# Performance work log

Hardware: AMD Instinct MI355X
Metric: run time of the kernel (lower is better)

## Reference

```python
import jax, jax.numpy as jnp
import numpy as np

B, T, E, H, HD, FF = 2, 2048, 1024, 16, 64, 4096
LN_EPS = 1e-5


def _ln(x, g, b):
    mu = jnp.mean(x, axis=-1, keepdims=True)
    var = jnp.var(x, axis=-1, keepdims=True)
    return (x - mu) * jax.lax.rsqrt(var + LN_EPS) * g + b


def setup_inputs() -> dict:
    key = jax.random.key(0)
    ks = jax.random.split(key, 8)
    s = 0.02
    return {
        "x": jax.random.normal(ks[0], (B, T, E), jnp.float32),
        "Wq": jax.random.normal(ks[1], (H, E, HD), jnp.float32) * s,
        "Wk": jax.random.normal(ks[2], (H, E, HD), jnp.float32) * s,
        "Wv": jax.random.normal(ks[3], (H, E, HD), jnp.float32) * s,
        "Wproj": jax.random.normal(ks[4], (E, E), jnp.float32) * s,
        "bproj": jnp.zeros((E,), jnp.float32),
        "W1": jax.random.normal(ks[5], (E, FF), jnp.float32) * s,
        "b1": jnp.zeros((FF,), jnp.float32),
        "W2": jax.random.normal(ks[6], (FF, E), jnp.float32) * s,
        "b2": jnp.zeros((E,), jnp.float32),
        "g1": jnp.ones((E,), jnp.float32),
        "be1": jnp.zeros((E,), jnp.float32),
        "g2": jnp.ones((E,), jnp.float32),
        "be2": jnp.zeros((E,), jnp.float32),
    }


def reference(x, Wq, Wk, Wv, Wproj, bproj, W1, b1, W2, b2, g1, be1, g2, be2):
    # --- pre-LN multi-head causal self-attention (dropout = eval/identity) ---
    h = _ln(x, g1, be1)  # [B,T,E]
    q = jnp.einsum('btd,hde->bhte', h, Wq)  # [B,H,T,HD]
    k = jnp.einsum('btd,hde->bhte', h, Wk)
    v = jnp.einsum('btd,hde->bhte', h, Wv)
    # NOTE: original code scales by C**-0.5 where C = embedding_dim (not head_size)
    scale = E ** (-0.5)
    wei = jnp.einsum('bhqe,bhke->bhqk', q, k) * scale  # [B,H,T,T]
    causal = jnp.tril(jnp.ones((T, T), dtype=bool))
    wei = jnp.where(causal, wei, -jnp.inf)
    attn = jax.nn.softmax(wei, axis=-1)
    o = jnp.einsum('bhqk,bhke->bhqe', attn, v)  # [B,H,T,HD]
    o = o.transpose(0, 2, 1, 3).reshape(B, T, E)  # concat heads
    o = o @ Wproj + bproj
    x = x + o
    # --- ReLU FFN ---
    h2 = _ln(x, g2, be2)
    f = jax.nn.relu(h2 @ W1 + b1) @ W2 + b2
    return x + f
```

## Files before the change

### kernel.cpp

```cpp
#include <hip/hip_runtime.h>
#include <hip/hip_bf16.h>
#include <stdint.h>

#define T_SEQ 2048
#define E_DIM 1024
#define H_NUM 16
#define HD_DIM 64
#define FF_DIM 4096
#define B_NUM 2
#define N_TOK (B_NUM * T_SEQ)

typedef unsigned short ushort_t;
typedef __bf16 bf16x8 __attribute__((ext_vector_type(8)));
typedef float f32x4 __attribute__((ext_vector_type(4)));

__device__ __forceinline__ float bf2f(ushort_t u) {
    return __uint_as_float(((unsigned)u) << 16);
}
__device__ __forceinline__ ushort_t f2bf(float f) {
    unsigned u = __float_as_uint(f);
    u += 0x7fffu + ((u >> 16) & 1u);
    return (ushort_t)(u >> 16);
}
__device__ __forceinline__ float bflo(unsigned u) { return __uint_as_float(u << 16); }
__device__ __forceinline__ float bfhi(unsigned u) { return __uint_as_float(u & 0xffff0000u); }

__device__ __forceinline__ void async_copy16(const ushort_t* g, ushort_t* l) {
    __builtin_amdgcn_global_load_lds(
        (__attribute__((address_space(1))) uint32_t*)(ushort_t*)g,
        (__attribute__((address_space(3))) uint32_t*)l, 16, 0, 0);
}

__global__ __launch_bounds__(256) void ln_kernel(const float* __restrict__ x,
                                                 const float* __restrict__ g,
                                                 const float* __restrict__ be,
                                                 ushort_t* __restrict__ out) {
    __shared__ float red[8];
    const int row = blockIdx.x, tid = threadIdx.x;
    const float* xr = x + (size_t)row * E_DIM;
    float4 v = ((const float4*)xr)[tid];
    float s = v.x + v.y + v.z + v.w;
    float sq = v.x * v.x + v.y * v.y + v.z * v.z + v.w * v.w;
    for (int off = 32; off; off >>= 1) {
        s += __shfl_xor(s, off);
        sq += __shfl_xor(sq, off);
    }
    const int wid = tid >> 6, lane = tid & 63;
    if (lane == 0) { red[wid] = s; red[4 + wid] = sq; }
    __syncthreads();
    s = red[0] + red[1] + red[2] + red[3];
    sq = red[4] + red[5] + red[6] + red[7];
    const float mean = s * (1.0f / E_DIM);
    const float var = sq * (1.0f / E_DIM) - mean * mean;
    const float rstd = rsqrtf(var + 1e-5f);
    float4 gv = ((const float4*)g)[tid];
    float4 bv = ((const float4*)be)[tid];
    unsigned o0 = f2bf((v.x - mean) * rstd * gv.x + bv.x);
    unsigned o1 = f2bf((v.y - mean) * rstd * gv.y + bv.y);
    unsigned o2 = f2bf((v.z - mean) * rstd * gv.z + bv.z);
    unsigned o3 = f2bf((v.w - mean) * rstd * gv.w + bv.w);
    uint2 w;
    w.x = o0 | (o1 << 16);
    w.y = o2 | (o3 << 16);
    ((uint2*)(out + (size_t)row * E_DIM))[tid] = w;
}

__global__ __launch_bounds__(256) void reduce_ln_kernel(const ushort_t* __restrict__ p0,
                                                        const ushort_t* __restrict__ p1,
                                                        const float* __restrict__ x,
                                                        const float* __restrict__ bias,
                                                        const float* __restrict__ g,
                                                        const float* __restrict__ be,
                                                        float* __restrict__ x1,
                                                        ushort_t* __restrict__ h2) {
    __shared__ float red[8];
    const int row = blockIdx.x, tid = threadIdx.x;
    uint2 u0 = ((const uint2*)(p0 + (size_t)row * E_DIM))[tid];
    uint2 u1 = ((const uint2*)(p1 + (size_t)row * E_DIM))[tid];
    float4 xv = ((const float4*)(x + (size_t)row * E_DIM))[tid];
    float4 bv = ((const float4*)bias)[tid];
    float4 v;
    v.x = xv.x + bv.x + bflo(u0.x) + bflo(u1.x);
    v.y = xv.y + bv.y + bfhi(u0.x) + bfhi(u1.x);
    v.z = xv.z + bv.z + bflo(u0.y) + bflo(u1.y);
    v.w = xv.w + bv.w + bfhi(u0.y) + bfhi(u1.y);
    ((float4*)(x1 + (size_t)row * E_DIM))[tid] = v;
    float s = v.x + v.y + v.z + v.w;
    float sq = v.x * v.x + v.y * v.y + v.z * v.z + v.w * v.w;
    for (int off = 32; off; off >>= 1) {
        s += __shfl_xor(s, off);
        sq += __shfl_xor(sq, off);
    }
    const int wid = tid >> 6, lane = tid & 63;
    if (lane == 0) { red[wid] = s; red[4 + wid] = sq; }
    __syncthreads();
    s = red[0] + red[1] + red[2] + red[3];
    sq = red[4] + red[5] + red[6] + red[7];
    const float mean = s * (1.0f / E_DIM);
    const float var = sq * (1.0f / E_DIM) - mean * mean;
    const float rstd = rsqrtf(var + 1e-5f);
    float4 gv = ((const float4*)g)[tid];
    float4 ev = ((const float4*)be)[tid];
    unsigned o0 = f2bf((v.x - mean) * rstd * gv.x + ev.x);
    unsigned o1 = f2bf((v.y - mean) * rstd * gv.y + ev.y);
    unsigned o2 = f2bf((v.z - mean) * rstd * gv.z + ev.z);
    unsigned o3 = f2bf((v.w - mean) * rstd * gv.w + ev.w);
    uint2 w;
    w.x = o0 | (o1 << 16);
    w.y = o2 | (o3 << 16);
    ((uint2*)(h2 + (size_t)row * E_DIM))[tid] = w;
}

__global__ __launch_bounds__(256) void reduce_out_kernel(const ushort_t* __restrict__ p0,
                                                         const ushort_t* __restrict__ p1,
                                                         const float* __restrict__ x1,
                                                         const float* __restrict__ bias,
                                                         float* __restrict__ out) {
    const int row = blockIdx.x, tid = threadIdx.x;
    uint2 u0 = ((const uint2*)(p0 + (size_t)row * E_DIM))[tid];
    uint2 u1 = ((const uint2*)(p1 + (size_t)row * E_DIM))[tid];
    float4 xv = ((const float4*)(x1 + (size_t)row * E_DIM))[tid];
    float4 bv = ((const float4*)bias)[tid];
    float4 v;
    v.x = xv.x + bv.x + bflo(u0.x) + bflo(u1.x);
    v.y = xv.y + bv.y + bfhi(u0.x) + bfhi(u1.x);
    v.z = xv.z + bv.z + bflo(u0.y) + bflo(u1.y);
    v.w = xv.w + bv.w + bfhi(u0.y) + bfhi(u1.y);
    ((float4*)(out + (size_t)row * E_DIM))[tid] = v;
}

__global__ __launch_bounds__(256) void transpose_all_kernel(const float* __restrict__ Wq,
                                                            const float* __restrict__ Wk,
                                                            const float* __restrict__ Wv,
                                                            const float* __restrict__ Wproj,
                                                            const float* __restrict__ W1,
                                                            const float* __restrict__ W2,
                                                            ushort_t* __restrict__ WqkvT,
                                                            ushort_t* __restrict__ WprojT,
                                                            ushort_t* __restrict__ W1T,
                                                            ushort_t* __restrict__ W2T) {
    __shared__ ushort_t tile[32][33];
    const int id = blockIdx.x;
    const float* in;
    ushort_t* out;
    int R, C, r0, c0;
    if (id < 3072) {
        const int z = id >> 6, rem = id & 63;
        const int m = z >> 4, hh = z & 15;
        in = ((m == 0) ? Wq : ((m == 1) ? Wk : Wv)) + (size_t)hh * E_DIM * HD_DIM;
        out = WqkvT + (size_t)(m * E_DIM + hh * HD_DIM) * E_DIM;
        R = E_DIM; C = HD_DIM;
        c0 = (rem & 1) * 32; r0 = (rem >> 1) * 32;
    } else if (id < 4096) {
        const int i = id - 3072;
        in = Wproj; out = WprojT; R = E_DIM; C = E_DIM;
        c0 = (i & 31) * 32; r0 = (i >> 5) * 32;
    } else if (id < 8192) {
        const int i = id - 4096;
        in = W1; out = W1T; R = E_DIM; C = FF_DIM;
        c0 = (i & 127) * 32; r0 = (i >> 7) * 32;
    } else {
        const int i = id - 8192;
        in = W2; out = W2T; R = FF_DIM; C = E_DIM;
        c0 = (i & 31) * 32; r0 = (i >> 5) * 32;
    }
    const int tx = threadIdx.x, ty = threadIdx.y;
#pragma unroll
    for (int i = 0; i < 32; i += 8) tile[ty + i][tx] = f2bf(in[(size_t)(r0 + ty + i) * C + (c0 + tx)]);
    __syncthreads();
#pragma unroll
    for (int i = 0; i < 32; i += 8) out[(size_t)(c0 + ty + i) * R + (r0 + tx)] = tile[tx][ty + i];
}

template <int MODE, int BK>
__global__ __launch_bounds__(256) void gemm_bt(const ushort_t* __restrict__ A,
                                               const ushort_t* __restrict__ BT,
                                               const float* __restrict__ bias,
                                               const float* __restrict__ resid,
                                               void* __restrict__ C0,
                                               ushort_t* __restrict__ C1,
                                               ushort_t* __restrict__ C2,
                                               int M, int N, int K, int lda) {
    __shared__ __align__(16) ushort_t lds_a[2][128 * BK];
    __shared__ __align__(16) ushort_t lds_b[2][128 * BK];
    const int tid = threadIdx.x;
    const int id = blockIdx.y * gridDim.x + blockIdx.x;
    const int band = id & 7, within = id >> 3;
    const int rpb = gridDim.y >> 3;
    const int by = band * rpb + (within % rpb);
    const int bx = within / rpb;
    const int m0 = by * 128, n0 = bx * 128;
    const int koff = blockIdx.z * K;
    const int wave = tid >> 6, lane = tid & 63;
    const int wm = (wave >> 1) * 64, wn = (wave & 1) * 64;
    const int quad = lane >> 4, l16 = lane & 15;
    f32x4 acc[4][4] = {};

    const int nk = K / BK;
    auto stage = [&](int kt, int buf) {
        const int k0 = koff + kt * BK;
#pragma unroll
        for (int it = 0; it < BK / 16; ++it) {
            const int ci = it * 256 + tid;
            const int kk = ci >> 9;
            const int rem = ci & 511;
            const int r = rem >> 2, kc = rem & 3;
            const int gk = k0 + kk * 32 + kc * 8;
            async_copy16(A + (size_t)(m0 + r) * lda + gk, &lds_a[buf][ci * 8]);
            async_copy16(BT + (size_t)(n0 + r) * lda + gk, &lds_b[buf][ci * 8]);
        }
    };
    stage(0, 0);

#pragma unroll 1
    for (int kt = 0; kt < nk; ++kt) {
        __syncthreads();
        if (kt + 1 < nk) stage(kt + 1, (kt + 1) & 1);
        const ushort_t* la = lds_a[kt & 1];
        const ushort_t* lb = lds_b[kt & 1];
#pragma unroll
        for (int kk = 0; kk < BK / 32; ++kk) {
            const ushort_t* lak = la + kk * 4096;
            const ushort_t* lbk = lb + kk * 4096;
            bf16x8 af[4], bfr[4];
#pragma unroll
            for (int i = 0; i < 4; i++) af[i] = *(const bf16x8*)&lak[(wm + i * 16 + l16) * 32 + quad * 8];
#pragma unroll
            for (int i = 0; i < 4; i++) bfr[i] = *(const bf16x8*)&lbk[(wn + i * 16 + l16) * 32 + quad * 8];
#pragma unroll
            for (int im = 0; im < 4; im++)
#pragma unroll
                for (int in = 0; in < 4; in++)
                    acc[im][in] = __builtin_amdgcn_mfma_f32_16x16x32_bf16(af[im], bfr[in], acc[im][in], 0, 0, 0);
        }
    }

    ushort_t* pc = nullptr;
    if (MODE == 3) pc = (blockIdx.z == 0) ? (ushort_t*)C0 : C1;
#pragma unroll
    for (int im = 0; im < 4; im++) {
#pragma unroll
        for (int in = 0; in < 4; in++) {
            const int col = n0 + wn + in * 16 + l16;
            float bv = (MODE == 1) ? bias[col] : 0.0f;
#pragma unroll
            for (int r = 0; r < 4; r++) {
                const int row = m0 + wm + im * 16 + quad * 4 + r;
                float v = acc[im][in][r] + bv;
                if (MODE == 1) {
                    v += resid[(size_t)row * N + col];
                    ((float*)C0)[(size_t)row * N + col] = v;
                } else {
                    pc[(size_t)row * N + col] = f2bf(v);
                }
            }
        }
    }
    (void)M; (void)C2;
}

template <int MODE>
__global__ __launch_bounds__(512, 2) void gemm256(const ushort_t* __restrict__ A,
                                                  const ushort_t* __restrict__ BT,
                                                  const float* __restrict__ bias,
                                                  void* __restrict__ C0,
                                                  ushort_t* __restrict__ C1,
                                                  ushort_t* __restrict__ C2,
                                                  int N, int K, int lda) {
    __shared__ __align__(16) ushort_t lds_a[2][16384];
    __shared__ __align__(16) ushort_t lds_b[2][16384];
    const int tid = threadIdx.x;
    const int id = blockIdx.y * gridDim.x + blockIdx.x;
    const int band = id & 7, within = id >> 3;
    const int rpb = gridDim.y >> 3;
    const int by = band * rpb + (within % rpb);
    const int bx = within / rpb;
    const int m0 = by * 256, n0 = bx * 256;
    const int wave = tid >> 6, lane = tid & 63;
    const int wr = wave >> 2, wc = wave & 3;
    const int quad = lane >> 4, l16 = lane & 15;
    const int nkt = K >> 6;

    f32x4 acc[8][4] = {};

    auto stageA = [&](int kt, int half) {
        ushort_t* dst = &lds_a[kt & 1][half * 8192];
        const ushort_t* src = A + (size_t)(m0 + half * 128) * lda + kt * 64;
#pragma unroll
        for (int it = 0; it < 2; ++it) {
            const int ci = it * 512 + tid;
            const int r = ci >> 3, c = ci & 7;
            async_copy16(src + (size_t)r * lda + ((c ^ (r & 7)) << 3), dst + ci * 8);
        }
    };
    auto stageB = [&](int kt, int half) {
        ushort_t* dst = &lds_b[kt & 1][half * 8192];
        const ushort_t* src = BT + (size_t)(n0 + half * 128) * lda + kt * 64;
#pragma unroll
        for (int it = 0; it < 2; ++it) {
            const int ci = it * 512 + tid;
            const int r = ci >> 3, c = ci & 7;
            async_copy16(src + (size_t)r * lda + ((c ^ (r & 7)) << 3), dst + ci * 8);
        }
    };

    stageA(0, 0); stageA(0, 1);
    stageB(0, 0); stageB(0, 1);
    stageB(1, 0); stageB(1, 1);
    asm volatile("s_waitcnt vmcnt(4)" ::: "memory");
    __builtin_amdgcn_s_barrier();

    const int swz = l16 & 7;

#pragma unroll 1
    for (int kt = 0; kt < nkt; ++kt) {
        const int buf = kt & 1;
        const ushort_t* la = &lds_a[buf][wr * 8192];
        const ushort_t* lb = &lds_b[buf][(wc >> 1) * 8192];
        const int brow = (wc & 1) * 64;
        bf16x8 bfrag[2][4];
#pragma unroll
        for (int p = 0; p < 4; ++p) {
            bf16x8 af[2][2];
#pragma unroll
            for (int s = 0; s < 2; ++s) {
                const int r = (p * 2 + s) * 16 + l16;
#pragma unroll
                for (int kk = 0; kk < 2; ++kk)
                    af[s][kk] = *(const bf16x8*)&la[r * 64 + (((kk << 2) + quad) ^ swz) * 8];
            }
            if (p == 0) {
#pragma unroll
                for (int kk = 0; kk < 2; ++kk)
#pragma unroll
                    for (int fn = 0; fn < 4; ++fn) {
                        const int r = brow + fn * 16 + l16;
                        bfrag[kk][fn] = *(const bf16x8*)&lb[r * 64 + (((kk << 2) + quad) ^ swz) * 8];
                    }
            }
            if (p == 0) { if (kt + 1 < nkt) stageA(kt + 1, 0); }
            else if (p == 1) { if (kt + 1 < nkt) stageA(kt + 1, 1); }
            else if (p == 2) { if (kt + 2 < nkt) stageB(kt + 2, 0); }
            else { if (kt + 2 < nkt) stageB(kt + 2, 1); }

            __builtin_amdgcn_s_barrier();
            asm volatile("s_waitcnt lgkmcnt(0)" ::: "memory");
            __builtin_amdgcn_sched_barrier(0);
            __builtin_amdgcn_s_setprio(1);
#pragma unroll
            for (int s = 0; s < 2; ++s)
#pragma unroll
                for (int kk = 0; kk < 2; ++kk)
#pragma unroll
                    for (int fn = 0; fn < 4; ++fn)
                        acc[p * 2 + s][fn] = __builtin_amdgcn_mfma_f32_16x16x32_bf16(
                            af[s][kk], bfrag[kk][fn], acc[p * 2 + s][fn], 0, 0, 0);
            __builtin_amdgcn_s_setprio(0);
            if (p == 3) {
                if (kt + 2 < nkt) asm volatile("s_waitcnt vmcnt(4)" ::: "memory");
                else              asm volatile("s_waitcnt vmcnt(0)" ::: "memory");
            }
            __builtin_amdgcn_s_barrier();
        }
    }

#pragma unroll
    for (int fm = 0; fm < 8; ++fm) {
        const int row_base = m0 + wr * 128 + fm * 16 + quad * 4;
#pragma unroll
        for (int fn = 0; fn < 4; ++fn) {
            const int col = n0 + wc * 64 + fn * 16 + l16;
            const float bv = bias[col];
#pragma unroll
            for (int r = 0; r < 4; ++r)
                ((ushort_t*)C0)[(size_t)(row_base + r) * N + col] =
                    f2bf(fmaxf(acc[fm][fn][r] + bv, 0.0f));
        }
    }
    (void)C1; (void)C2;
}

__global__ __launch_bounds__(512, 2) void gemm192_qkv(const ushort_t* __restrict__ A,
                                                      const ushort_t* __restrict__ BT,
                                                      ushort_t* __restrict__ qP,
                                                      ushort_t* __restrict__ kP,
                                                      ushort_t* __restrict__ vP,
                                                      int K, int lda) {
    __shared__ __align__(16) ushort_t lds_a[2][16384];
    __shared__ __align__(16) ushort_t lds_b[2][12288];
    const int tid = threadIdx.x;
    const int id = blockIdx.y * gridDim.x + blockIdx.x;
    const int band = id & 7, within = id >> 3;
    const int rpb = gridDim.y >> 3;
    const int by = band * rpb + (within % rpb);
    const int bx = within / rpb;
    const int m0 = by * 256, n0 = bx * 192;
    const int wave = tid >> 6, lane = tid & 63;
    const int wr = wave >> 2, wc = wave & 3;
    const int quad = lane >> 4, l16 = lane & 15;
    const int nkt = K >> 6;

    f32x4 acc[8][3] = {};

    auto stageA = [&](int kt, int half) {
        ushort_t* dst = &lds_a[kt & 1][half * 8192];
        const ushort_t* src = A + (size_t)(m0 + half * 128) * lda + kt * 64;
#pragma unroll
        for (int it = 0; it < 2; ++it) {
            const int ci = it * 512 + tid;
            const int r = ci >> 3, c = ci & 7;
            async_copy16(src + (size_t)r * lda + ((c ^ (r & 7)) << 3), dst + ci * 8);
        }
    };
    auto stageB = [&](int kt) {
        ushort_t* dst = lds_b[kt & 1];
        const ushort_t* src = BT + (size_t)n0 * lda + kt * 64;
#pragma unroll
        for (int it = 0; it < 3; ++it) {
            const int ci = it * 512 + tid;
            const int r = ci >> 3, c = ci & 7;
            async_copy16(src + (size_t)r * lda + ((c ^ (r & 7)) << 3), dst + ci * 8);
        }
    };

    stageA(0, 0); stageA(0, 1);
    stageB(0);
    stageB(1);
    asm volatile("s_waitcnt vmcnt(3)" ::: "memory");
    __builtin_amdgcn_s_barrier();

    const int swz = l16 & 7;

#pragma unroll 1
    for (int kt = 0; kt < nkt; ++kt) {
        const int buf = kt & 1;
        const ushort_t* la = &lds_a[buf][wr * 8192];
        const ushort_t* lb = lds_b[buf];
        const int brow = wc * 48;
        bf16x8 bfrag[2][3];
#pragma unroll
        for (int p = 0; p < 4; ++p) {
            bf16x8 af[2][2];
#pragma unroll
            for (int s = 0; s < 2; ++s) {
                const int r = (p * 2 + s) * 16 + l16;
#pragma unroll
                for (int kk = 0; kk < 2; ++kk)
                    af[s][kk] = *(const bf16x8*)&la[r * 64 + (((kk << 2) + quad) ^ swz) * 8];
            }
            if (p == 0) {
#pragma unroll
                for (int kk = 0; kk < 2; ++kk)
#pragma unroll
                    for (int fn = 0; fn < 3; ++fn) {
                        const int r = brow + fn * 16 + l16;
                        bfrag[kk][fn] = *(const bf16x8*)&lb[r * 64 + (((kk << 2) + quad) ^ swz) * 8];
                    }
            }
            if (p == 0) { if (kt + 1 < nkt) stageA(kt + 1, 0); }
            else if (p == 1) { if (kt + 1 < nkt) stageA(kt + 1, 1); }
            else if (p == 2) { if (kt + 2 < nkt) stageB(kt + 2); }

            __builtin_amdgcn_s_barrier();
            asm volatile("s_waitcnt lgkmcnt(0)" ::: "memory");
            __builtin_amdgcn_sched_barrier(0);
            __builtin_amdgcn_s_setprio(1);
#pragma unroll
            for (int s = 0; s < 2; ++s)
#pragma unroll
                for (int kk = 0; kk < 2; ++kk)
#pragma unroll
                    for (int fn = 0; fn < 3; ++fn)
                        acc[p * 2 + s][fn] = __builtin_amdgcn_mfma_f32_16x16x32_bf16(
                            af[s][kk], bfrag[kk][fn], acc[p * 2 + s][fn], 0, 0, 0);
            __builtin_amdgcn_s_setprio(0);
            if (p == 3) {
                if (kt + 2 < nkt) asm volatile("s_waitcnt vmcnt(3)" ::: "memory");
                else              asm volatile("s_waitcnt vmcnt(0)" ::: "memory");
            }
            __builtin_amdgcn_s_barrier();
        }
    }

#pragma unroll
    for (int fm = 0; fm < 8; ++fm) {
        const int row_base = m0 + wr * 128 + fm * 16 + quad * 4;
#pragma unroll
        for (int fn = 0; fn < 3; ++fn) {
            const int col = n0 + wc * 48 + fn * 16 + l16;
            const int mat = col >> 10, c = col & 1023, hh = c >> 6, d = c & 63;
#pragma unroll
            for (int r = 0; r < 4; ++r) {
                const int row = row_base + r;
                const int bb = row >> 11, tt = row & 2047;
                const int bh = bb * H_NUM + hh;
                float v = acc[fm][fn][r];
                size_t idx;
                ushort_t* dst;
                if (mat == 0) {
                    idx = ((((size_t)bh * 32 + (tt >> 6)) * 8 + (d >> 3)) * 64 + (tt & 63)) * 8 + (d & 7);
                    dst = qP;
                    v *= 0.0450842048f;
                } else if (mat == 1) {
                    idx = ((((size_t)bh * 32 + (tt >> 6)) * 8 + (d >> 3)) * 64 + (tt & 63)) * 8 + (d & 7);
                    dst = kP;
                } else {
                    idx = ((((size_t)bh * 32 + (tt >> 6)) * 8 + ((tt & 63) >> 3)) * 64 + d) * 8 + (tt & 7);
                    dst = vP;
                }
                dst[idx] = f2bf(v);
            }
        }
    }
}

__global__ __launch_bounds__(256, 2) void attn_flash(const ushort_t* __restrict__ qP,
                                                     const ushort_t* __restrict__ kP,
                                                     const ushort_t* __restrict__ vP,
                                                     ushort_t* __restrict__ o) {
    __shared__ __align__(16) ushort_t P_lds[4][32 * 72];
    __shared__ __align__(16) float Ored[2][32][68];
    __shared__ float Lred[2][32];
    const int h = blockIdx.x, p = blockIdx.y, b = blockIdx.z;
    const int bh = b * H_NUM + h;
    const int tid = threadIdx.x;
    const int wave = tid >> 6, lane = tid & 63;
    const int wr = wave >> 1, ws = wave & 1;
    const int quad = lane >> 4, l16 = lane & 15;
    ushort_t* Pw = P_lds[wave];
    const ushort_t* kbase = kP + (size_t)bh * 32 * 4096;
    const ushort_t* vbase = vP + (size_t)bh * 32 * 4096;
    bf16x8 onesf;
#pragma unroll
    for (int j = 0; j < 8; ++j) onesf[j] = (__bf16)1.0f;

#pragma unroll 1
    for (int phase = 0; phase < 2; ++phase) {
        const int qt = (phase == 0) ? (31 - p) : p;
        const int nkt = qt + 1;
        const ushort_t* qbase = qP + ((size_t)bh * 32 + qt) * 4096;
        bf16x8 qf[2][2];
#pragma unroll
        for (int rg = 0; rg < 2; ++rg)
#pragma unroll
            for (int kk = 0; kk < 2; ++kk)
                qf[rg][kk] = *(const bf16x8*)&qbase[((kk * 4 + quad) * 64 + wr * 32 + rg * 16 + l16) * 8];
        f32x4 oacc[2][4] = {};
        f32x4 lacc[2] = {};
        __syncthreads();
        bf16x8 kf[8], vf[8];
        {
            const ushort_t* kb = kbase + (size_t)ws * 4096;
#pragma unroll
            for (int i = 0; i < 8; ++i)
                kf[i] = *(const bf16x8*)&kb[(((i >> 2) * 4 + quad) * 64 + (i & 3) * 16 + l16) * 8];
        }
#pragma unroll 1
        for (int kt = ws; kt < nkt; kt += 2) {
            f32x4 sacc[2][4] = {};
            __builtin_amdgcn_s_setprio(1);
#pragma unroll
            for (int kk = 0; kk < 2; ++kk)
#pragma unroll
                for (int kg = 0; kg < 4; ++kg)
#pragma unroll
                    for (int rg = 0; rg < 2; ++rg)
                        sacc[rg][kg] = __builtin_amdgcn_mfma_f32_16x16x32_bf16(
                            qf[rg][kk], kf[kk * 4 + kg], sacc[rg][kg], 0, 0, 0);
            __builtin_amdgcn_s_setprio(0);
            {
                const ushort_t* vb = vbase + (size_t)kt * 4096;
#pragma unroll
                for (int i = 0; i < 8; ++i)
                    vf[i] = *(const bf16x8*)&vb[(((i >> 2) * 4 + quad) * 64 + (i & 3) * 16 + l16) * 8];
            }
            if (kt + 2 < nkt) {
                const ushort_t* kb = kbase + (size_t)(kt + 2) * 4096;
#pragma unroll
                for (int i = 0; i < 8; ++i)
                    kf[i] = *(const bf16x8*)&kb[(((i >> 2) * 4 + quad) * 64 + (i & 3) * 16 + l16) * 8];
            }
#pragma unroll
            for (int rg = 0; rg < 2; ++rg)
#pragma unroll
                for (int kg = 0; kg < 4; ++kg) {
                    f32x4 sv = sacc[rg][kg];
                    if (kt == qt) {
                        const int jc = kg * 16 + l16;
#pragma unroll
                        for (int r = 0; r < 4; ++r)
                            if (jc > wr * 32 + rg * 16 + quad * 4 + r) sv[r] = -3.0e38f;
                    }
#pragma unroll
                    for (int r = 0; r < 4; ++r) {
                        const float e = exp2f(sv[r]);
                        Pw[(rg * 16 + quad * 4 + r) * 72 + kg * 16 + l16] =
                            (ushort_t)(__float_as_uint(e) >> 16);
                    }
                }
            __builtin_amdgcn_s_setprio(1);
#pragma unroll
            for (int kk = 0; kk < 2; ++kk)
#pragma unroll
                for (int rg = 0; rg < 2; ++rg) {
                    bf16x8 pf = *(const bf16x8*)&Pw[(rg * 16 + l16) * 72 + kk * 32 + quad * 8];
                    lacc[rg] = __builtin_amdgcn_mfma_f32_16x16x32_bf16(pf, onesf, lacc[rg], 0, 0, 0);
#pragma unroll
                    for (int dg = 0; dg < 4; ++dg)
                        oacc[rg][dg] = __builtin_amdgcn_mfma_f32_16x16x32_bf16(
                            pf, vf[kk * 4 + dg], oacc[rg][dg], 0, 0, 0);
                }
            __builtin_amdgcn_s_setprio(0);
        }
        if (ws == 1) {
#pragma unroll
            for (int rg = 0; rg < 2; ++rg) {
#pragma unroll
                for (int dg = 0; dg < 4; ++dg)
#pragma unroll
                    for (int r = 0; r < 4; ++r)
                        Ored[wr][rg * 16 + quad * 4 + r][dg * 16 + l16] = oacc[rg][dg][r];
                if (l16 == 0) {
#pragma unroll
                    for (int r = 0; r < 4; ++r)
                        Lred[wr][rg * 16 + quad * 4 + r] = lacc[rg][r];
                }
            }
        }
        __syncthreads();
        if (ws == 0) {
#pragma unroll
            for (int rg = 0; rg < 2; ++rg)
#pragma unroll
                for (int r = 0; r < 4; ++r) {
                    const int rr = rg * 16 + quad * 4 + r;
                    const float inv = 1.0f / (lacc[rg][r] + Lred[wr][rr]);
                    const int trow = qt * 64 + wr * 32 + rr;
#pragma unroll
                    for (int dg = 0; dg < 4; ++dg) {
                        const float v = oacc[rg][dg][r] + Ored[wr][rr][dg * 16 + l16];
                        o[(size_t)(b * T_SEQ + trow) * E_DIM + h * HD_DIM + dg * 16 + l16] =
                            f2bf(v * inv);
                    }
                }
        }
    }
}

extern "C" void kernel_launch(void* const* d_in, const int* in_sizes, int n_in,
                              void* d_out, int out_size, void* d_ws, size_t ws_size,
                              hipStream_t stream) {
    const float* x = (const float*)d_in[0];
    const float* Wq = (const float*)d_in[1];
    const float* Wk = (const float*)d_in[2];
    const float* Wv = (const float*)d_in[3];
    const float* Wproj = (const float*)d_in[4];
    const float* bproj = (const float*)d_in[5];
    const float* W1 = (const float*)d_in[6];
    const float* b1 = (const float*)d_in[7];
    const float* W2 = (const float*)d_in[8];
    const float* b2 = (const float*)d_in[9];
    const float* g1 = (const float*)d_in[10];
    const float* be1 = (const float*)d_in[11];
    const float* g2 = (const float*)d_in[12];
    const float* be2 = (const float*)d_in[13];

    char* ws = (char*)d_ws;
    const size_t MB = 1024 * 1024;
    ushort_t* W2T    = (ushort_t*)(ws + 0 * MB);
    float*    x1     = (float*)   (ws + 8 * MB);
    ushort_t* W1T    = (ushort_t*)(ws + 24 * MB);
    ushort_t* WprojT = (ushort_t*)(ws + 32 * MB);
    ushort_t* hln    = (ushort_t*)(ws + 34 * MB);
    ushort_t* ocat   = hln;
    ushort_t* WqkvT  = (ushort_t*)(ws + 42 * MB);
    ushort_t* qP     = (ushort_t*)(ws + 48 * MB);
    ushort_t* kP     = (ushort_t*)(ws + 56 * MB);
    ushort_t* vP     = (ushort_t*)(ws + 64 * MB);
    ushort_t* h2     = (ushort_t*)(ws + 72 * MB);
    ushort_t* f1     = (ushort_t*)(ws + 34 * MB);
    ushort_t* pp0    = (ushort_t*)(ws + 48 * MB);
    ushort_t* pp1    = (ushort_t*)(ws + 56 * MB);
    ushort_t* fp0    = (ushort_t*)(ws + 66 * MB);
    ushort_t* fp1    = (ushort_t*)(ws + 24 * MB);
    (void)ws_size; (void)in_sizes; (void)n_in; (void)out_size;

    transpose_all_kernel<<<12288, dim3(32, 8, 1), 0, stream>>>(
        Wq, Wk, Wv, Wproj, W1, W2, WqkvT, WprojT, W1T, W2T);

    ln_kernel<<<N_TOK, 256, 0, stream>>>(x, g1, be1, hln);
    gemm192_qkv<<<dim3(16, 16), 512, 0, stream>>>(hln, WqkvT, qP, kP, vP, E_DIM, E_DIM);
    attn_flash<<<dim3(16, 16, 2), 256, 0, stream>>>(qP, kP, vP, ocat);
    gemm_bt<3, 64><<<dim3(8, 32, 2), 256, 0, stream>>>(ocat, WprojT, nullptr, nullptr,
                                                       pp0, pp1, nullptr, N_TOK, E_DIM, 512, E_DIM);
    reduce_ln_kernel<<<N_TOK, 256, 0, stream>>>(pp0, pp1, x, bproj, g2, be2, x1, h2);
    gemm256<2><<<dim3(16, 16), 512, 0, stream>>>(h2, W1T, b1, f1, nullptr, nullptr,
                                                 FF_DIM, E_DIM, E_DIM);
    gemm_bt<3, 64><<<dim3(8, 32, 2), 256, 0, stream>>>(f1, W2T, nullptr, nullptr,
                                                       fp0, fp1, nullptr, N_TOK, E_DIM, 2048, FF_DIM);
    reduce_out_kernel<<<N_TOK, 256, 0, stream>>>(fp0, fp1, x1, b2, (float*)d_out);
}
```

Baseline: 316.7 us.

## Replace split-K 128x128 GEMM with swizzled 256x128 pipelined kernel for projections

The output projection and second FFN GEMM (both split-K by 2) move from the simple 128x128 double-buffered kernel to a new 512-thread 256x128 tile kernel. It uses XOR-swizzled LDS layouts, staggered async staging of A halves and B across phases, priority raising around MFMA blocks, and explicit waitcnt/barrier scheduling. The grid shrinks from 512 to 256 blocks, trading fewer blocks for more reuse per tile and better load/compute overlap. The unused templated gemm256 is also specialised into a non-template FFN1 kernel.

```diff
diff --git a/kernel.cpp b/kernel.cpp
--- a/kernel.cpp
+++ b/kernel.cpp
@@ -172,101 +172,11 @@
     for (int i = 0; i < 32; i += 8) out[(size_t)(c0 + ty + i) * R + (r0 + tx)] = tile[tx][ty + i];
 }
 
-template <int MODE, int BK>
-__global__ __launch_bounds__(256) void gemm_bt(const ushort_t* __restrict__ A,
-                                               const ushort_t* __restrict__ BT,
-                                               const float* __restrict__ bias,
-                                               const float* __restrict__ resid,
-                                               void* __restrict__ C0,
-                                               ushort_t* __restrict__ C1,
-                                               ushort_t* __restrict__ C2,
-                                               int M, int N, int K, int lda) {
-    __shared__ __align__(16) ushort_t lds_a[2][128 * BK];
-    __shared__ __align__(16) ushort_t lds_b[2][128 * BK];
-    const int tid = threadIdx.x;
-    const int id = blockIdx.y * gridDim.x + blockIdx.x;
-    const int band = id & 7, within = id >> 3;
-    const int rpb = gridDim.y >> 3;
-    const int by = band * rpb + (within % rpb);
-    const int bx = within / rpb;
-    const int m0 = by * 128, n0 = bx * 128;
-    const int koff = blockIdx.z * K;
-    const int wave = tid >> 6, lane = tid & 63;
-    const int wm = (wave >> 1) * 64, wn = (wave & 1) * 64;
-    const int quad = lane >> 4, l16 = lane & 15;
-    f32x4 acc[4][4] = {};
-
-    const int nk = K / BK;
-    auto stage = [&](int kt, int buf) {
-        const int k0 = koff + kt * BK;
-#pragma unroll
-        for (int it = 0; it < BK / 16; ++it) {
-            const int ci = it * 256 + tid;
-            const int kk = ci >> 9;
-            const int rem = ci & 511;
-            const int r = rem >> 2, kc = rem & 3;
-            const int gk = k0 + kk * 32 + kc * 8;
-            async_copy16(A + (size_t)(m0 + r) * lda + gk, &lds_a[buf][ci * 8]);
-            async_copy16(BT + (size_t)(n0 + r) * lda + gk, &lds_b[buf][ci * 8]);
-        }
-    };
-    stage(0, 0);
-
-#pragma unroll 1
-    for (int kt = 0; kt < nk; ++kt) {
-        __syncthreads();
-        if (kt + 1 < nk) stage(kt + 1, (kt + 1) & 1);
-        const ushort_t* la = lds_a[kt & 1];
-        const ushort_t* lb = lds_b[kt & 1];
-#pragma unroll
-        for (int kk = 0; kk < BK / 32; ++kk) {
-            const ushort_t* lak = la + kk * 4096;
-            const ushort_t* lbk = lb + kk * 4096;
-            bf16x8 af[4], bfr[4];
-#pragma unroll
-            for (int i = 0; i < 4; i++) af[i] = *(const bf16x8*)&lak[(wm + i * 16 + l16) * 32 + quad * 8];
-#pragma unroll
-            for (int i = 0; i < 4; i++) bfr[i] = *(const bf16x8*)&lbk[(wn + i * 16 + l16) * 32 + quad * 8];
-#pragma unroll
-            for (int im = 0; im < 4; im++)
-#pragma unroll
-                for (int in = 0; in < 4; in++)
-                    acc[im][in] = __builtin_amdgcn_mfma_f32_16x16x32_bf16(af[im], bfr[in], acc[im][in], 0, 0, 0);
-        }
-    }
-
-    ushort_t* pc = nullptr;
-    if (MODE == 3) pc = (blockIdx.z == 0) ? (ushort_t*)C0 : C1;
-#pragma unroll
-    for (int im = 0; im < 4; im++) {
-#pragma unroll
-        for (int in = 0; in < 4; in++) {
-            const int col = n0 + wn + in * 16 + l16;
-            float bv = (MODE == 1) ? bias[col] : 0.0f;
-#pragma unroll
-            for (int r = 0; r < 4; r++) {
-                const int row = m0 + wm + im * 16 + quad * 4 + r;
-                float v = acc[im][in][r] + bv;
-                if (MODE == 1) {
-                    v += resid[(size_t)row * N + col];
-                    ((float*)C0)[(size_t)row * N + col] = v;
-                } else {
-                    pc[(size_t)row * N + col] = f2bf(v);
-                }
-            }
-        }
-    }
-    (void)M; (void)C2;
-}
-
-template <int MODE>
-__global__ __launch_bounds__(512, 2) void gemm256(const ushort_t* __restrict__ A,
-                                                  const ushort_t* __restrict__ BT,
-                                                  const float* __restrict__ bias,
-                                                  void* __restrict__ C0,
-                                                  ushort_t* __restrict__ C1,
-                                                  ushort_t* __restrict__ C2,
-                                                  int N, int K, int lda) {
+__global__ __launch_bounds__(512, 2) void gemm256_ffn1(const ushort_t* __restrict__ A,
+                                                       const ushort_t* __restrict__ BT,
+                                                       const float* __restrict__ bias,
+                                                       ushort_t* __restrict__ C,
+                                                       int N, int K, int lda) {
     __shared__ __align__(16) ushort_t lds_a[2][16384];
     __shared__ __align__(16) ushort_t lds_b[2][16384];
     const int tid = threadIdx.x;
@@ -373,11 +283,10 @@
             const float bv = bias[col];
 #pragma unroll
             for (int r = 0; r < 4; ++r)
-                ((ushort_t*)C0)[(size_t)(row_base + r) * N + col] =
+                C[(size_t)(row_base + r) * N + col] =
                     f2bf(fmaxf(acc[fm][fn][r] + bv, 0.0f));
         }
     }
-    (void)C1; (void)C2;
 }
 
 __global__ __launch_bounds__(512, 2) void gemm192_qkv(const ushort_t* __restrict__ A,
@@ -514,6 +423,122 @@
     }
 }
 
+__global__ __launch_bounds__(512, 2) void gemm128n(const ushort_t* __restrict__ A,
+                                                   const ushort_t* __restrict__ BT,
+                                                   ushort_t* __restrict__ P0,
+                                                   ushort_t* __restrict__ P1,
+                                                   int N, int K, int lda) {
+    __shared__ __align__(16) ushort_t lds_a[2][16384];
+    __shared__ __align__(16) ushort_t lds_b[2][8192];
+    const int tid = threadIdx.x;
+    const int id = blockIdx.y * gridDim.x + blockIdx.x;
+    const int band = id & 7, within = id >> 3;
+    const int rpb = gridDim.y >> 3;
+    const int by = band * rpb + (within % rpb);
+    const int bx = within / rpb;
+    const int m0 = by * 256, n0 = bx * 128;
+    const int koff = blockIdx.z * K;
+    const int wave = tid >> 6, lane = tid & 63;
+    const int wr = wave >> 2, wc = wave & 3;
+    const int quad = lane >> 4, l16 = lane & 15;
+    const int nkt = K >> 6;
+
+    f32x4 acc[8][2] = {};
+
+    auto stageA = [&](int kt, int half) {
+        ushort_t* dst = &lds_a[kt & 1][half * 8192];
+        const ushort_t* src = A + (size_t)(m0 + half * 128) * lda + koff + kt * 64;
+#pragma unroll
+        for (int it = 0; it < 2; ++it) {
+            const int ci = it * 512 + tid;
+            const int r = ci >> 3, c = ci & 7;
+            async_copy16(src + (size_t)r * lda + ((c ^ (r & 7)) << 3), dst + ci * 8);
+        }
+    };
+    auto stageB = [&](int kt) {
+        ushort_t* dst = lds_b[kt & 1];
+        const ushort_t* src = BT + (size_t)n0 * lda + koff + kt * 64;
+#pragma unroll
+        for (int it = 0; it < 2; ++it) {
+            const int ci = it * 512 + tid;
+            const int r = ci >> 3, c = ci & 7;
+            async_copy16(src + (size_t)r * lda + ((c ^ (r & 7)) << 3), dst + ci * 8);
+        }
+    };
+
+    stageA(0, 0); stageA(0, 1);
+    stageB(0);
+    stageB(1);
+    asm volatile("s_waitcnt vmcnt(2)" ::: "memory");
+    __builtin_amdgcn_s_barrier();
+
+    const int swz = l16 & 7;
+
+#pragma unroll 1
+    for (int kt = 0; kt < nkt; ++kt) {
+        const int buf = kt & 1;
+        const ushort_t* la = &lds_a[buf][wr * 8192];
+        const ushort_t* lb = lds_b[buf];
+        const int brow = wc * 32;
+        bf16x8 bfrag[2][2];
+#pragma unroll
+        for (int p = 0; p < 4; ++p) {
+            bf16x8 af[2][2];
+#pragma unroll
+            for (int s = 0; s < 2; ++s) {
+                const int r = (p * 2 + s) * 16 + l16;
+#pragma unroll
+                for (int kk = 0; kk < 2; ++kk)
+                    af[s][kk] = *(const bf16x8*)&la[r * 64 + (((kk << 2) + quad) ^ swz) * 8];
+            }
+            if (p == 0) {
+#pragma unroll
+                for (int kk = 0; kk < 2; ++kk)
+#pragma unroll
+                    for (int fn = 0; fn < 2; ++fn) {
+                        const int r = brow + fn * 16 + l16;
+                        bfrag[kk][fn] = *(const bf16x8*)&lb[r * 64 + (((kk << 2) + quad) ^ swz) * 8];
+                    }
+            }
+            if (p == 0) { if (kt + 1 < nkt) stageA(kt + 1, 0); }
+            else if (p == 1) { if (kt + 1 < nkt) stageA(kt + 1, 1); }
+            else if (p == 2) { if (kt + 2 < nkt) stageB(kt + 2); }
+
+            __builtin_amdgcn_s_barrier();
+            asm volatile("s_waitcnt lgkmcnt(0)" ::: "memory");
+            __builtin_amdgcn_sched_barrier(0);
+            __builtin_amdgcn_s_setprio(1);
+#pragma unroll
+            for (int s = 0; s < 2; ++s)
+#pragma unroll
+                for (int kk = 0; kk < 2; ++kk)
+#pragma unroll
+                    for (int fn = 0; fn < 2; ++fn)
+                        acc[p * 2 + s][fn] = __builtin_amdgcn_mfma_f32_16x16x32_bf16(
+                            af[s][kk], bfrag[kk][fn], acc[p * 2 + s][fn], 0, 0, 0);
+            __builtin_amdgcn_s_setprio(0);
+            if (p == 3) {
+                if (kt + 2 < nkt) asm volatile("s_waitcnt vmcnt(2)" ::: "memory");
+                else              asm volatile("s_waitcnt vmcnt(0)" ::: "memory");
+            }
+            __builtin_amdgcn_s_barrier();
+        }
+    }
+
+    ushort_t* pc = (blockIdx.z == 0) ? P0 : P1;
+#pragma unroll
+    for (int fm = 0; fm < 8; ++fm) {
+        const int row_base = m0 + wr * 128 + fm * 16 + quad * 4;
+#pragma unroll
+        for (int fn = 0; fn < 2; ++fn) {
+            const int col = n0 + wc * 32 + fn * 16 + l16;
+#pragma unroll
+            for (int r = 0; r < 4; ++r)
+                pc[(size_t)(row_base + r) * N + col] = f2bf(acc[fm][fn][r]);
+        }
+    }
+}
+
 __global__ __launch_bounds__(256, 2) void attn_flash(const ushort_t* __restrict__ qP,
                                                      const ushort_t* __restrict__ kP,
                                                      const ushort_t* __restrict__ vP,
@@ -691,12 +716,11 @@
     ln_kernel<<<N_TOK, 256, 0, stream>>>(x, g1, be1, hln);
     gemm192_qkv<<<dim3(16, 16), 512, 0, stream>>>(hln, WqkvT, qP, kP, vP, E_DIM, E_DIM);
     attn_flash<<<dim3(16, 16, 2), 256, 0, stream>>>(qP, kP, vP, ocat);
-    gemm_bt<3, 64><<<dim3(8, 32, 2), 256, 0, stream>>>(ocat, WprojT, nullptr, nullptr,
-                                                       pp0, pp1, nullptr, N_TOK, E_DIM, 512, E_DIM);
+    gemm128n<<<dim3(8, 16, 2), 512, 0, stream>>>(ocat, WprojT, pp0, pp1,
+                                                 E_DIM, 512, E_DIM);
     reduce_ln_kernel<<<N_TOK, 256, 0, stream>>>(pp0, pp1, x, bproj, g2, be2, x1, h2);
-    gemm256<2><<<dim3(16, 16), 512, 0, stream>>>(h2, W1T, b1, f1, nullptr, nullptr,
-                                                 FF_DIM, E_DIM, E_DIM);
-    gemm_bt<3, 64><<<dim3(8, 32, 2), 256, 0, stream>>>(f1, W2T, nullptr, nullptr,
-                                                       fp0, fp1, nullptr, N_TOK, E_DIM, 2048, FF_DIM);
+    gemm256_ffn1<<<dim3(16, 16), 512, 0, stream>>>(h2, W1T, b1, f1, FF_DIM, E_DIM, E_DIM);
+    gemm128n<<<dim3(8, 16, 2), 512, 0, stream>>>(f1, W2T, fp0, fp1,
+                                                 E_DIM, 2048, FF_DIM);
     reduce_out_kernel<<<N_TOK, 256, 0, stream>>>(fp0, fp1, x1, b2, (float*)d_out);
 }
```

After: 327.6 us. 1.03x slower.
